# Optimization experiments

Hardware: AMD Instinct MI355X
Metric: run time of the kernel (lower is better)

## Reference

```python
import jax, jax.numpy as jnp
import numpy as np

N_HEADS = 2
WINDOW = 4
BLOCK = 256


def _get_rel_emb(emb, length):
    # emb: [1, 2*WINDOW+1, K] -> [1, 2*length-1, K]
    pad = max(length - (WINDOW + 1), 0)
    start = max((WINDOW + 1) - length, 0)
    e = jnp.pad(emb, ((0, 0), (pad, pad), (0, 0)))
    return e[:, start:start + 2 * length - 1]


def _rel_to_abs(x):
    # x: [b, h, l, 2l-1] -> [b, h, l, l] (skew trick)
    b, h, l, _ = x.shape
    x = jnp.pad(x, ((0, 0), (0, 0), (0, 0), (0, 1))).reshape(b, h, 2 * l * l)
    x = jnp.pad(x, ((0, 0), (0, 0), (0, l - 1))).reshape(b, h, l + 1, 2 * l - 1)
    return x[:, :, :l, l - 1:]


def _abs_to_rel(x):
    # x: [b, h, l, l] -> [b, h, l, 2l-1] (inverse skew)
    b, h, l, _ = x.shape
    x = jnp.pad(x, ((0, 0), (0, 0), (0, 0), (0, l - 1))).reshape(b, h, l * (2 * l - 1))
    x = jnp.pad(x, ((0, 0), (0, 0), (l, 0))).reshape(b, h, l, 2 * l)
    return x[:, :, :, 1:]


def _attention(x, c, attn_mask, Wq, bq, Wk, bk, Wv, bv, Wo, bo, emb_rel_k, emb_rel_v):
    B, C, T = x.shape
    H, K = N_HEADS, C // N_HEADS
    # projections (torch Linear on [B,T,C])
    q = (jnp.einsum('bct,cd->btd', x, Wq) + bq).reshape(B, T, H, K).transpose(0, 2, 1, 3)
    k = (jnp.einsum('bct,cd->btd', c, Wk) + bk).reshape(B, T, H, K).transpose(0, 2, 1, 3)
    v = (jnp.einsum('bct,cd->btd', c, Wv) + bv).reshape(B, T, H, K).transpose(0, 2, 1, 3)
    qs = q / jnp.sqrt(jnp.float32(K))
    scores = jnp.einsum('bhtk,bhsk->bhts', qs, k)  # [B,H,T,T]
    # relative-position key logits (heads_share=True -> single table)
    rel_k = _get_rel_emb(emb_rel_k, T)[0]          # [2T-1, K]
    rel_logits = jnp.einsum('bhtk,rk->bhtr', qs, rel_k)
    scores = scores + _rel_to_abs(rel_logits)
    # proximal bias: -log1p(|i-j|)
    r = jnp.arange(T, dtype=jnp.float32)
    scores = scores - jnp.log1p(jnp.abs(r[:, None] - r[None, :]))[None, None]
    # attn mask + block-local mask (block mask active because mask is given)
    ij = jnp.arange(T)
    block_ok = jnp.abs(ij[:, None] - ij[None, :]) <= BLOCK
    valid = (attn_mask != 0) & block_ok[None, None]
    scores = jnp.where(valid, scores, jnp.float32(-1e4))
    p = jax.nn.softmax(scores, axis=-1)
    out = jnp.einsum('bhts,bhsk->bhtk', p, v)
    # relative-position value contribution
    rel_v = _get_rel_emb(emb_rel_v, T)[0]          # [2T-1, K]
    out = out + jnp.einsum('bhtr,rk->bhtk', _abs_to_rel(p), rel_v)
    out = out.transpose(0, 2, 1, 3).reshape(B, T, C)
    y = jnp.einsum('btd,do->bto', out, Wo) + bo
    return y.transpose(0, 2, 1)  # [B, out_channels, T]


def setup_inputs() -> dict:
    key = jax.random.key(0)
    ks = jax.random.split(key, 8)
    B, C, T = 4, 192, 2048
    K = C // N_HEADS
    s = jnp.float32(0.05)
    rel_std = jnp.float32(K ** -0.5)
    return {
        'x': jax.random.normal(ks[0], (B, C, T), jnp.float32),
        'c': jax.random.normal(ks[1], (B, C, T), jnp.float32),
        'Wq': jax.random.normal(ks[2], (C, C), jnp.float32) * s,
        'bq': jnp.zeros((C,), jnp.float32),
        'Wk': jax.random.normal(ks[3], (C, C), jnp.float32) * s,
        'bk': jnp.zeros((C,), jnp.float32),
        'Wv': jax.random.normal(ks[4], (C, C), jnp.float32) * s,
        'bv': jnp.zeros((C,), jnp.float32),
        'Wo': jax.random.normal(ks[5], (C, C), jnp.float32) * s,
        'bo': jnp.zeros((C,), jnp.float32),
        'emb_rel_k': jax.random.normal(ks[6], (1, 2 * WINDOW + 1, K), jnp.float32) * rel_std,
        'emb_rel_v': jax.random.normal(ks[7], (1, 2 * WINDOW + 1, K), jnp.float32) * rel_std,
        'attn_mask': jnp.ones((B, 1, T, T), jnp.int32),
    }


def reference(x, c, Wq, bq, Wk, bk, Wv, bv, Wo, bo, emb_rel_k, emb_rel_v, attn_mask):
    return _attention(x, c, attn_mask, Wq, bq, Wk, bk, Wv, bv, Wo, bo, emb_rel_k, emb_rel_v)
```

## Files before the change

kernel.cpp:

```cpp
#include <hip/hip_runtime.h>
#include <hip/hip_bf16.h>

#define B_DIM 4
#define C_DIM 192
#define T_SEQ 2048
#define H_DIM 2
#define K_DIM 96
#define BAND 256
#define IT 16
#define NJT 34
#define WSLOT 544
#define WPD 556
#define PRS (2*WPD)
#define PMW 17
#define XSTR 200
#define OSTR 200
#define PDS 40

typedef __attribute__((ext_vector_type(8))) short bf16x8;
typedef __attribute__((ext_vector_type(4))) short bf16x4;
typedef __attribute__((ext_vector_type(4))) float f32x4;
#define MFMA16 __builtin_amdgcn_mfma_f32_16x16x32_bf16

__device__ __forceinline__ float bfbits2f(short s) {
    union { short s; __hip_bfloat16 h; } u; u.s = s; return __bfloat162float(u.h);
}
__device__ __forceinline__ short f2bf_bits(float f) {
    union { __hip_bfloat16 h; short s; } u; u.h = __float2bfloat16(f); return u.s;
}

#define OFF_WT(m)  ((size_t)(m)*73728)
#define OFF_BQS    ((size_t)294912)
#define OFF_RELKBF ((size_t)295680)
#define OFF_RVT    ((size_t)298752)
#define OFF_QBF    ((size_t)304896)
#define OFF_KBF    (OFF_QBF + 3145728)
#define OFF_VTB    (OFF_KBF + 3145728)

__device__ __forceinline__ int swz512(int hw) { return ((hw & 7) << 6) + (hw >> 3); }

__global__ __launch_bounds__(256)
void prep_kernel(const float* __restrict__ Wq, const float* __restrict__ Wk,
                 const float* __restrict__ Wv, const float* __restrict__ Wo,
                 const float* __restrict__ bq, const float* __restrict__ relk,
                 const float* __restrict__ relv, char* __restrict__ ws)
{
    const float qscale = 0.10206207261596577f;
    const int bidx = blockIdx.x;
    const int tid  = threadIdx.x;

    if (bidx < 576) {
        const size_t idx = (size_t)bidx*256 + tid;
        const int mi  = (int)(idx / 36864);
        const int rem = (int)(idx % 36864);
        const int c = rem / C_DIM, d = rem % C_DIM;
        const float* src = (mi == 0) ? Wq : (mi == 1) ? Wk : (mi == 2) ? Wv : Wo;
        float v = src[c*C_DIM + d];
        if (mi == 0) v *= qscale;
        ((short*)(ws + OFF_WT(mi)))[d*C_DIM + c] = f2bf_bits(v);
        return;
    }
    if (tid < C_DIM)
        ((float*)(ws + OFF_BQS))[tid] = bq[tid]*qscale;
    short* rkb = (short*)(ws + OFF_RELKBF);
    for (int idx = tid; idx < 16*K_DIM; idx += 256) {
        const int row = idx / K_DIM;
        rkb[idx] = (row < 9) ? f2bf_bits(relk[idx]) : (short)0;
    }
    short* rvt = (short*)(ws + OFF_RVT);
    for (int idx = tid; idx < K_DIM*32; idx += 256) {
        const int col = idx >> 5, dd = idx & 31;
        rvt[idx] = (dd < 9) ? f2bf_bits(relv[dd*K_DIM + col]) : (short)0;
    }
}

__global__ __launch_bounds__(256)
void proj_kernel(const float* __restrict__ x, const float* __restrict__ cin,
                 const float* __restrict__ bk, const float* __restrict__ bv,
                 char* __restrict__ ws)
{
    __shared__ short xs[IT*XSTR];
    __shared__ short cs[IT*XSTR];
    const int bid = swz512(blockIdx.x);
    const int b   = bid >> 7;
    const int t0  = (bid & 127) * IT;
    const int tid = threadIdx.x;
    const int wave = tid >> 6, lane = tid & 63;
    const int q4 = lane >> 4, lr = lane & 15;

    for (int l = tid; l < 768; l += 256) {
        const int cr = l >> 2, u = l & 3;
        const size_t off = (size_t)(b*C_DIM + cr)*T_SEQ + t0 + 4*u;
        const float4 xv = *reinterpret_cast<const float4*>(x + off);
        const float4 cv = *reinterpret_cast<const float4*>(cin + off);
        xs[(4*u+0)*XSTR + cr] = f2bf_bits(xv.x);
        xs[(4*u+1)*XSTR + cr] = f2bf_bits(xv.y);
        xs[(4*u+2)*XSTR + cr] = f2bf_bits(xv.z);
        xs[(4*u+3)*XSTR + cr] = f2bf_bits(xv.w);
        cs[(4*u+0)*XSTR + cr] = f2bf_bits(cv.x);
        cs[(4*u+1)*XSTR + cr] = f2bf_bits(cv.y);
        cs[(4*u+2)*XSTR + cr] = f2bf_bits(cv.z);
        cs[(4*u+3)*XSTR + cr] = f2bf_bits(cv.w);
    }
    __syncthreads();

    const short* WqT = (const short*)(ws + OFF_WT(0));
    const short* WkT = (const short*)(ws + OFF_WT(1));
    const short* WvT = (const short*)(ws + OFF_WT(2));

    f32x4 qa[3], ka[3], va[3];
    #pragma unroll
    for (int j = 0; j < 3; ++j) {
        qa[j] = (f32x4){0,0,0,0}; ka[j] = (f32x4){0,0,0,0}; va[j] = (f32x4){0,0,0,0};
    }
    for (int kc = 0; kc < 6; ++kc) {
        const int ko = kc*32 + q4*8;
        const bf16x8 xf = *reinterpret_cast<const bf16x8*>(xs + lr*XSTR + ko);
        const bf16x8 cf = *reinterpret_cast<const bf16x8*>(cs + lr*XSTR + ko);
        #pragma unroll
        for (int j = 0; j < 3; ++j) {
            const int dt = 3*wave + j;
            const bf16x8 wqf = *reinterpret_cast<const bf16x8*>(WqT + (dt*16 + lr)*C_DIM + ko);
            const bf16x8 wkf = *reinterpret_cast<const bf16x8*>(WkT + (dt*16 + lr)*C_DIM + ko);
            const bf16x8 wvf = *reinterpret_cast<const bf16x8*>(WvT + (dt*16 + lr)*C_DIM + ko);
            qa[j] = MFMA16(xf, wqf, qa[j], 0, 0, 0);
            ka[j] = MFMA16(cf, wkf, ka[j], 0, 0, 0);
            va[j] = MFMA16(wvf, cf, va[j], 0, 0, 0);
        }
    }

    const float* bqs = (const float*)(ws + OFF_BQS);
    short* qbf = (short*)(ws + OFF_QBF);
    short* kbf = (short*)(ws + OFF_KBF);
    short* vtb = (short*)(ws + OFF_VTB);
    #pragma unroll
    for (int j = 0; j < 3; ++j) {
        const int dt = 3*wave + j;
        {
            const int d = dt*16 + lr, h = d/K_DIM, kk = d%K_DIM;
            const int bh = b*H_DIM + h;
            const float bq_v = bqs[d], bk_v = bk[d];
            #pragma unroll
            for (int e = 0; e < 4; ++e) {
                const int t = t0 + q4*4 + e;
                const size_t off = ((size_t)bh*T_SEQ + t)*K_DIM + kk;
                qbf[off] = f2bf_bits(qa[j][e] + bq_v);
                kbf[off] = f2bf_bits(ka[j][e] + bk_v);
            }
        }
        {
            #pragma unroll
            for (int e = 0; e < 4; ++e) {
                const int d = dt*16 + q4*4 + e, h = d/K_DIM, kk = d%K_DIM;
                const int bh = b*H_DIM + h;
                vtb[((size_t)bh*K_DIM + kk)*T_SEQ + t0 + lr] = f2bf_bits(va[e == e ? j : j][e] + bv[d]);
            }
        }
    }
}

__global__ __launch_bounds__(512, 4)
void attn_oproj_kernel(const int* __restrict__ mask, const float* __restrict__ bo,
                       float* __restrict__ y, char* __restrict__ ws)
{
    __shared__ __align__(16) float ps[2*IT*WPD];
    __shared__ float lt[257];
    __shared__ __align__(16) char upool[2560];
    unsigned* pm_s = (unsigned*)upool;
    float*    rl   = (float*)(upool + 1088);
    short*    pd_s = (short*)upool;

    const short* qbf = (const short*)(ws + OFF_QBF);
    const short* kbf = (const short*)(ws + OFF_KBF);
    const short* vtb = (const short*)(ws + OFF_VTB);
    const short* rkb = (const short*)(ws + OFF_RELKBF);
    const short* rvt = (const short*)(ws + OFF_RVT);
    const short* WoT = (const short*)(ws + OFF_WT(3));

    const int bid = swz512(blockIdx.x);
    const int b   = bid >> 7;
    const int i0  = (bid & 127) * IT;
    const int tid = threadIdx.x;
    const int wave = tid >> 6, lane = tid & 63;
    const int head = wave >> 2, wv = wave & 3;
    const int q4 = lane >> 4, lr = lane & 15;

    const int jlo  = max(0, i0 - BAND);
    const int jhi  = min(T_SEQ - 1, i0 + IT - 1 + BAND);
    const int wlen = jhi - jlo + 1;
    const size_t qk_base = (size_t)(b*H_DIM + head) * T_SEQ * K_DIM;

    bf16x8 qa[3];
    {
        const short* qrow = qbf + qk_base + (size_t)(i0 + lr)*K_DIM + q4*8;
        #pragma unroll
        for (int kc = 0; kc < 3; ++kc)
            qa[kc] = *reinterpret_cast<const bf16x8*>(qrow + kc*32);
    }

    for (int idx = tid; idx < 257; idx += 512) lt[idx] = log1pf((float)idx);

    if (tid < IT*PMW) {
        const int r = tid / PMW, w = tid % PMW;
        const int* mrow = mask + ((size_t)b*T_SEQ + i0 + r)*T_SEQ;
        unsigned bits = 0;
        #pragma unroll
        for (int g4 = 0; g4 < 8; ++g4) {
            const int jg = jlo + 32*w + 4*g4;
            if (jg + 3 < T_SEQ) {
                const int4 mv = *reinterpret_cast<const int4*>(mrow + jg);
                bits |= (unsigned)(mv.x != 0) << (4*g4);
                bits |= (unsigned)(mv.y != 0) << (4*g4+1);
                bits |= (unsigned)(mv.z != 0) << (4*g4+2);
                bits |= (unsigned)(mv.w != 0) << (4*g4+3);
            } else {
                #pragma unroll
                for (int e = 0; e < 4; ++e)
                    if (jg + e < T_SEQ && mrow[jg+e] != 0) bits |= 1u << (4*g4+e);
            }
        }
        pm_s[tid] = bits;
    }

    float* psh = ps + head*(IT*WPD);
    {
        int jt = wv;
        int jr = jlo + jt*16 + lr; if (jr > T_SEQ-1) jr = T_SEQ-1;
        const short* kr = kbf + qk_base + (size_t)jr*K_DIM + q4*8;
        bf16x8 kf0 = *reinterpret_cast<const bf16x8*>(kr);
        bf16x8 kf1 = *reinterpret_cast<const bf16x8*>(kr + 32);
        bf16x8 kf2 = *reinterpret_cast<const bf16x8*>(kr + 64);
        while (true) {
            const int jn = jt + 4;
            const bool more = (jn < NJT);
            bf16x8 nf0, nf1, nf2;
            if (more) {
                int jr2 = jlo + jn*16 + lr; if (jr2 > T_SEQ-1) jr2 = T_SEQ-1;
                const short* kr2 = kbf + qk_base + (size_t)jr2*K_DIM + q4*8;
                nf0 = *reinterpret_cast<const bf16x8*>(kr2);
                nf1 = *reinterpret_cast<const bf16x8*>(kr2 + 32);
                nf2 = *reinterpret_cast<const bf16x8*>(kr2 + 64);
            }
            f32x4 s = {0.f,0.f,0.f,0.f};
            s = MFMA16(qa[0], kf0, s, 0, 0, 0);
            s = MFMA16(qa[1], kf1, s, 0, 0, 0);
            s = MFMA16(qa[2], kf2, s, 0, 0, 0);
            float* pr = psh + (q4*4)*WPD + jt*16 + lr;
            pr[0*WPD] = s[0]; pr[1*WPD] = s[1]; pr[2*WPD] = s[2]; pr[3*WPD] = s[3];
            if (!more) break;
            kf0 = nf0; kf1 = nf1; kf2 = nf2;
            jt = jn;
        }
    }
    if (wv == 3) {
        const short* krow = rkb + lr*K_DIM + q4*8;
        f32x4 rs = {0.f,0.f,0.f,0.f};
        #pragma unroll
        for (int kc = 0; kc < 3; ++kc)
            rs = MFMA16(qa[kc], *reinterpret_cast<const bf16x8*>(krow + kc*32), rs, 0, 0, 0);
        if (lr < 9) {
            #pragma unroll
            for (int e = 0; e < 4; ++e)
                rl[head*144 + (q4*4 + e)*9 + lr] = rs[e];
        }
    }
    __syncthreads();

    {
        const int rg = tid >> 4, sj = tid & 15;
        const int hh = rg >> 4, r = rg & 15;
        const int i = i0 + r;
        float* prow = ps + hh*(IT*WPD) + r*WPD;
        float vals[36];
        float m = -INFINITY;
        #pragma unroll
        for (int mm = 0; mm < 9; ++mm) {
            const int j0 = 4*sj + 64*mm;
            float4 pv = make_float4(0.f,0.f,0.f,0.f);
            unsigned mb = 0;
            if (j0 < WSLOT) {
                pv = *reinterpret_cast<const float4*>(prow + j0);
                mb = pm_s[r*PMW + (j0 >> 5)] >> (j0 & 31);
            }
            const float pe[4] = {pv.x, pv.y, pv.z, pv.w};
            #pragma unroll
            for (int e = 0; e < 4; ++e) {
                const int j = j0 + e;
                float val = -INFINITY;
                if (j0 < WSLOT && j < wlen) {
                    const int jg = jlo + j, dd = jg - i;
                    const int ad = dd < 0 ? -dd : dd;
                    if (ad <= BAND && ((mb >> e) & 1)) {
                        val = pe[e] - lt[ad];
                        if ((unsigned)(dd + 4) <= 8u) val += rl[hh*144 + r*9 + dd + 4];
                    }
                }
                vals[mm*4 + e] = val;
                m = fmaxf(m, val);
            }
        }
        #pragma unroll
        for (int off = 8; off > 0; off >>= 1) m = fmaxf(m, __shfl_xor(m, off, 64));
        if (m == -INFINITY) m = 0.f;
        float ssum = 0.f;
        #pragma unroll
        for (int u = 0; u < 36; ++u) { vals[u] = __expf(vals[u] - m); ssum += vals[u]; }
        #pragma unroll
        for (int off = 8; off > 0; off >>= 1) ssum += __shfl_xor(ssum, off, 64);
        const float inv = ssum > 0.f ? 1.f/ssum : 0.f;
        short* pbrow = (short*)prow;
        #pragma unroll
        for (int mm = 0; mm < 9; ++mm) {
            const int j0 = 4*sj + 64*mm;
            if (j0 < WSLOT) {
                bf16x4 w;
                #pragma unroll
                for (int e = 0; e < 4; ++e) w[e] = f2bf_bits(vals[mm*4+e]*inv);
                *reinterpret_cast<bf16x4*>(pbrow + j0) = w;
            }
        }
    }
    __syncthreads();

    for (int idx = tid; idx < 2*IT*PDS; idx += 512) {
        const int hh = idx / (IT*PDS), rem2 = idx % (IT*PDS);
        const int r = rem2 / PDS, kk = rem2 % PDS;
        short v = 0;
        if (kk < 9) {
            const int jg = i0 + r + kk - 4;
            if (jg >= 0 && jg < T_SEQ)
                v = ((const short*)ps)[hh*(IT*PRS) + r*PRS + (jg - jlo)];
        }
        pd_s[idx] = v;
    }

    const short* pbh = (const short*)ps + head*(IT*PRS);
    f32x4 o0 = {0.f,0.f,0.f,0.f}, o1 = {0.f,0.f,0.f,0.f};
    {
        const short* vbase0 = vtb + qk_base + (size_t)(wv*16 + lr)*T_SEQ;
        const short* vbase1 = vtb + qk_base + (size_t)((wv+4)*16 + lr)*T_SEQ;
        int tc = jlo + q4*8; if (tc > T_SEQ-8) tc = T_SEQ-8;
        bf16x8 vb0 = *reinterpret_cast<const bf16x8*>(vbase0 + tc);
        bf16x8 vb1 = {};
        if (wv < 2) vb1 = *reinterpret_cast<const bf16x8*>(vbase1 + tc);
        for (int kc = 0; kc < NJT/2; ++kc) {
            bf16x8 nv0, nv1;
            const bool more = (kc + 1 < NJT/2);
            if (more) {
                int tn = jlo + (kc+1)*32 + q4*8; if (tn > T_SEQ-8) tn = T_SEQ-8;
                nv0 = *reinterpret_cast<const bf16x8*>(vbase0 + tn);
                if (wv < 2) nv1 = *reinterpret_cast<const bf16x8*>(vbase1 + tn);
            }
            const bf16x8 pa = *reinterpret_cast<const bf16x8*>(pbh + lr*PRS + kc*32 + q4*8);
            o0 = MFMA16(pa, vb0, o0, 0, 0, 0);
            if (wv < 2) o1 = MFMA16(pa, vb1, o1, 0, 0, 0);
            if (more) { vb0 = nv0; if (wv < 2) vb1 = nv1; }
        }
    }
    __syncthreads();

    {
        const bf16x8 pda = *reinterpret_cast<const bf16x8*>(pd_s + head*(IT*PDS) + lr*PDS + q4*8);
        const bf16x8 rv0 = *reinterpret_cast<const bf16x8*>(rvt + (wv*16 + lr)*32 + q4*8);
        o0 = MFMA16(pda, rv0, o0, 0, 0, 0);
        if (wv < 2) {
            const bf16x8 rv1 = *reinterpret_cast<const bf16x8*>(rvt + ((wv+4)*16 + lr)*32 + q4*8);
            o1 = MFMA16(pda, rv1, o1, 0, 0, 0);
        }
    }

    {
        short* outs = (short*)ps;
        #pragma unroll
        for (int u = 0; u < 2; ++u) {
            if (u == 1 && wv >= 2) break;
            const int nt = u ? wv + 4 : wv;
            const f32x4 oc = u ? o1 : o0;
            const int col = head*K_DIM + nt*16 + lr;
            #pragma unroll
            for (int e = 0; e < 4; ++e)
                outs[(q4*4 + e)*OSTR + col] = f2bf_bits(oc[e]);
        }
    }
    __syncthreads();

    {
        const short* outs = (const short*)ps;
        #pragma unroll
        for (int u = 0; u < 2; ++u) {
            if (u == 1 && wave >= 4) break;
            const int dt = u ? wave + 8 : wave;
            f32x4 a = {0.f,0.f,0.f,0.f};
            #pragma unroll
            for (int kc = 0; kc < 6; ++kc) {
                const int ko = kc*32 + q4*8;
                const bf16x8 af = *reinterpret_cast<const bf16x8*>(
                    WoT + (size_t)(dt*16 + lr)*C_DIM + ko);
                const bf16x8 bfr = *reinterpret_cast<const bf16x8*>(outs + lr*OSTR + ko);
                a = MFMA16(af, bfr, a, 0, 0, 0);
            }
            #pragma unroll
            for (int e = 0; e < 4; ++e) {
                const int d = dt*16 + q4*4 + e;
                y[((size_t)b*C_DIM + d)*T_SEQ + i0 + lr] = a[e] + bo[d];
            }
        }
    }
}

extern "C" void kernel_launch(void* const* d_in, const int* in_sizes, int n_in,
                              void* d_out, int out_size, void* d_ws, size_t ws_size,
                              hipStream_t stream)
{
    const float* x    = (const float*)d_in[0];
    const float* c    = (const float*)d_in[1];
    const float* Wq   = (const float*)d_in[2];
    const float* bq   = (const float*)d_in[3];
    const float* Wk   = (const float*)d_in[4];
    const float* bk   = (const float*)d_in[5];
    const float* Wv   = (const float*)d_in[6];
    const float* bv   = (const float*)d_in[7];
    const float* Wo   = (const float*)d_in[8];
    const float* bo   = (const float*)d_in[9];
    const float* relk = (const float*)d_in[10];
    const float* relv = (const float*)d_in[11];
    const int*   mask = (const int*)d_in[12];
    float*       y    = (float*)d_out;
    char*        ws   = (char*)d_ws;

    hipLaunchKernelGGL(prep_kernel, dim3(577), dim3(256), 0, stream,
                       Wq, Wk, Wv, Wo, bq, relk, relv, ws);
    hipLaunchKernelGGL(proj_kernel, dim3(B_DIM*(T_SEQ/16)), dim3(256), 0, stream,
                       x, c, bk, bv, ws);
    hipLaunchKernelGGL(attn_oproj_kernel, dim3(B_DIM*(T_SEQ/IT)), dim3(512), 0, stream,
                       mask, bo, y, ws);
}
```

Baseline: 175.3 us.

## Split attention per head, separate output projection, and split QKV projection blocks

The fused attention plus output-projection kernel becomes a per-head attention kernel with 256 threads that writes bf16 head outputs to a workspace buffer, followed by a separate output-projection kernel. The QKV projection is split into three blocks per tile, one per matrix, which triples the grid and lowers per-block register use. Weight transposition in prep now goes through a shared-memory tile so global reads and writes are coalesced. The aim is more parallel blocks and better occupancy, at the cost of an extra launch and a round trip of the attention output through global memory.

Result: slower. 183.9 us (+4.9%).

```diff
diff --git a/kernel.cpp b/kernel.cpp
--- a/kernel.cpp
+++ b/kernel.cpp
@@ -14,7 +14,6 @@
 #define PRS (2*WPD)
 #define PMW 17
 #define XSTR 200
-#define OSTR 200
 #define PDS 40
 
 typedef __attribute__((ext_vector_type(8))) short bf16x8;
@@ -22,9 +21,6 @@
 typedef __attribute__((ext_vector_type(4))) float f32x4;
 #define MFMA16 __builtin_amdgcn_mfma_f32_16x16x32_bf16
 
-__device__ __forceinline__ float bfbits2f(short s) {
-    union { short s; __hip_bfloat16 h; } u; u.s = s; return __bfloat162float(u.h);
-}
 __device__ __forceinline__ short f2bf_bits(float f) {
     union { __hip_bfloat16 h; short s; } u; u.h = __float2bfloat16(f); return u.s;
 }
@@ -36,8 +32,7 @@
 #define OFF_QBF    ((size_t)304896)
 #define OFF_KBF    (OFF_QBF + 3145728)
 #define OFF_VTB    (OFF_KBF + 3145728)
-
-__device__ __forceinline__ int swz512(int hw) { return ((hw & 7) << 6) + (hw >> 3); }
+#define OFF_OBTC   (OFF_VTB + 3145728)
 
 __global__ __launch_bounds__(256)
 void prep_kernel(const float* __restrict__ Wq, const float* __restrict__ Wk,
@@ -49,15 +44,26 @@
     const int bidx = blockIdx.x;
     const int tid  = threadIdx.x;
 
-    if (bidx < 576) {
-        const size_t idx = (size_t)bidx*256 + tid;
-        const int mi  = (int)(idx / 36864);
-        const int rem = (int)(idx % 36864);
-        const int c = rem / C_DIM, d = rem % C_DIM;
+    if (bidx < 144) {
+        __shared__ float tile[32][33];
+        const int mi = bidx / 36, tl = bidx % 36;
+        const int R0 = (tl / 6) * 32, C0 = (tl % 6) * 32;
         const float* src = (mi == 0) ? Wq : (mi == 1) ? Wk : (mi == 2) ? Wv : Wo;
-        float v = src[c*C_DIM + d];
-        if (mi == 0) v *= qscale;
-        ((short*)(ws + OFF_WT(mi)))[d*C_DIM + c] = f2bf_bits(v);
+        const int r = tid >> 5, cc = tid & 31;
+        #pragma unroll
+        for (int i = 0; i < 4; ++i) {
+            const int rr = r + 8*i;
+            tile[rr][cc] = src[(R0 + rr)*C_DIM + C0 + cc];
+        }
+        __syncthreads();
+        short* dst = (short*)(ws + OFF_WT(mi));
+        #pragma unroll
+        for (int i = 0; i < 4; ++i) {
+            const int rr = r + 8*i;
+            float v = tile[cc][rr];
+            if (mi == 0) v *= qscale;
+            dst[(C0 + rr)*C_DIM + R0 + cc] = f2bf_bits(v);
+        }
         return;
     }
     if (tid < C_DIM)
@@ -74,98 +80,82 @@
     }
 }
 
-__global__ __launch_bounds__(256)
+__global__ __launch_bounds__(256, 6)
 void proj_kernel(const float* __restrict__ x, const float* __restrict__ cin,
                  const float* __restrict__ bk, const float* __restrict__ bv,
                  char* __restrict__ ws)
 {
-    __shared__ short xs[IT*XSTR];
-    __shared__ short cs[IT*XSTR];
-    const int bid = swz512(blockIdx.x);
-    const int b   = bid >> 7;
-    const int t0  = (bid & 127) * IT;
+    __shared__ short sb[IT*XSTR];
+    const int hw = blockIdx.x;
+    const int L  = (hw & 7)*192 + (hw >> 3);
+    const int which = L % 3;
+    const int rest  = L / 3;
+    const int b  = rest >> 7;
+    const int t0 = (rest & 127) * IT;
     const int tid = threadIdx.x;
     const int wave = tid >> 6, lane = tid & 63;
     const int q4 = lane >> 4, lr = lane & 15;
 
+    const float* src = (which == 0) ? x : cin;
     for (int l = tid; l < 768; l += 256) {
         const int cr = l >> 2, u = l & 3;
-        const size_t off = (size_t)(b*C_DIM + cr)*T_SEQ + t0 + 4*u;
-        const float4 xv = *reinterpret_cast<const float4*>(x + off);
-        const float4 cv = *reinterpret_cast<const float4*>(cin + off);
-        xs[(4*u+0)*XSTR + cr] = f2bf_bits(xv.x);
-        xs[(4*u+1)*XSTR + cr] = f2bf_bits(xv.y);
-        xs[(4*u+2)*XSTR + cr] = f2bf_bits(xv.z);
-        xs[(4*u+3)*XSTR + cr] = f2bf_bits(xv.w);
-        cs[(4*u+0)*XSTR + cr] = f2bf_bits(cv.x);
-        cs[(4*u+1)*XSTR + cr] = f2bf_bits(cv.y);
-        cs[(4*u+2)*XSTR + cr] = f2bf_bits(cv.z);
-        cs[(4*u+3)*XSTR + cr] = f2bf_bits(cv.w);
+        const float4 v4 = *reinterpret_cast<const float4*>(
+            src + (size_t)(b*C_DIM + cr)*T_SEQ + t0 + 4*u);
+        sb[(4*u+0)*XSTR + cr] = f2bf_bits(v4.x);
+        sb[(4*u+1)*XSTR + cr] = f2bf_bits(v4.y);
+        sb[(4*u+2)*XSTR + cr] = f2bf_bits(v4.z);
+        sb[(4*u+3)*XSTR + cr] = f2bf_bits(v4.w);
     }
     __syncthreads();
 
-    const short* WqT = (const short*)(ws + OFF_WT(0));
-    const short* WkT = (const short*)(ws + OFF_WT(1));
-    const short* WvT = (const short*)(ws + OFF_WT(2));
-
-    f32x4 qa[3], ka[3], va[3];
+    const short* WT = (const short*)(ws + OFF_WT(which));
+    f32x4 a[3];
     #pragma unroll
-    for (int j = 0; j < 3; ++j) {
-        qa[j] = (f32x4){0,0,0,0}; ka[j] = (f32x4){0,0,0,0}; va[j] = (f32x4){0,0,0,0};
-    }
+    for (int j = 0; j < 3; ++j) a[j] = (f32x4){0.f,0.f,0.f,0.f};
     for (int kc = 0; kc < 6; ++kc) {
         const int ko = kc*32 + q4*8;
-        const bf16x8 xf = *reinterpret_cast<const bf16x8*>(xs + lr*XSTR + ko);
-        const bf16x8 cf = *reinterpret_cast<const bf16x8*>(cs + lr*XSTR + ko);
+        const bf16x8 sf = *reinterpret_cast<const bf16x8*>(sb + lr*XSTR + ko);
         #pragma unroll
         for (int j = 0; j < 3; ++j) {
-            const int dt = 3*wave + j;
-            const bf16x8 wqf = *reinterpret_cast<const bf16x8*>(WqT + (dt*16 + lr)*C_DIM + ko);
-            const bf16x8 wkf = *reinterpret_cast<const bf16x8*>(WkT + (dt*16 + lr)*C_DIM + ko);
-            const bf16x8 wvf = *reinterpret_cast<const bf16x8*>(WvT + (dt*16 + lr)*C_DIM + ko);
-            qa[j] = MFMA16(xf, wqf, qa[j], 0, 0, 0);
-            ka[j] = MFMA16(cf, wkf, ka[j], 0, 0, 0);
-            va[j] = MFMA16(wvf, cf, va[j], 0, 0, 0);
+            const bf16x8 wf = *reinterpret_cast<const bf16x8*>(
+                WT + ((3*wave + j)*16 + lr)*C_DIM + ko);
+            a[j] = (which == 2) ? MFMA16(wf, sf, a[j], 0, 0, 0)
+                                : MFMA16(sf, wf, a[j], 0, 0, 0);
         }
     }
 
     const float* bqs = (const float*)(ws + OFF_BQS);
-    short* qbf = (short*)(ws + OFF_QBF);
-    short* kbf = (short*)(ws + OFF_KBF);
-    short* vtb = (short*)(ws + OFF_VTB);
     #pragma unroll
     for (int j = 0; j < 3; ++j) {
         const int dt = 3*wave + j;
-        {
+        if (which <= 1) {
             const int d = dt*16 + lr, h = d/K_DIM, kk = d%K_DIM;
             const int bh = b*H_DIM + h;
-            const float bq_v = bqs[d], bk_v = bk[d];
+            const float bias = (which == 0) ? bqs[d] : bk[d];
+            short* dst = (short*)(ws + (which == 0 ? OFF_QBF : OFF_KBF));
             #pragma unroll
             for (int e = 0; e < 4; ++e) {
                 const int t = t0 + q4*4 + e;
-                const size_t off = ((size_t)bh*T_SEQ + t)*K_DIM + kk;
-                qbf[off] = f2bf_bits(qa[j][e] + bq_v);
-                kbf[off] = f2bf_bits(ka[j][e] + bk_v);
-            }
-        }
-        {
+                dst[((size_t)bh*T_SEQ + t)*K_DIM + kk] = f2bf_bits(a[j][e] + bias);
+            }
+        } else {
+            short* vtb = (short*)(ws + OFF_VTB);
             #pragma unroll
             for (int e = 0; e < 4; ++e) {
                 const int d = dt*16 + q4*4 + e, h = d/K_DIM, kk = d%K_DIM;
                 const int bh = b*H_DIM + h;
-                vtb[((size_t)bh*K_DIM + kk)*T_SEQ + t0 + lr] = f2bf_bits(va[e == e ? j : j][e] + bv[d]);
-            }
-        }
-    }
-}
-
-__global__ __launch_bounds__(512, 4)
-void attn_oproj_kernel(const int* __restrict__ mask, const float* __restrict__ bo,
-                       float* __restrict__ y, char* __restrict__ ws)
+                vtb[((size_t)bh*K_DIM + kk)*T_SEQ + t0 + lr] = f2bf_bits(a[j][e] + bv[d]);
+            }
+        }
+    }
+}
+
+__global__ __launch_bounds__(256, 4)
+void attn_kernel(const int* __restrict__ mask, char* __restrict__ ws)
 {
-    __shared__ __align__(16) float ps[2*IT*WPD];
+    __shared__ __align__(16) float ps[IT*WPD];
     __shared__ float lt[257];
-    __shared__ __align__(16) char upool[2560];
+    __shared__ __align__(16) char upool[1664];
     unsigned* pm_s = (unsigned*)upool;
     float*    rl   = (float*)(upool + 1088);
     short*    pd_s = (short*)upool;
@@ -175,14 +165,15 @@
     const short* vtb = (const short*)(ws + OFF_VTB);
     const short* rkb = (const short*)(ws + OFF_RELKBF);
     const short* rvt = (const short*)(ws + OFF_RVT);
-    const short* WoT = (const short*)(ws + OFF_WT(3));
-
-    const int bid = swz512(blockIdx.x);
-    const int b   = bid >> 7;
-    const int i0  = (bid & 127) * IT;
+    short* obtc = (short*)(ws + OFF_OBTC);
+
+    const int L    = ((blockIdx.x & 7) << 7) + (blockIdx.x >> 3);
+    const int b    = L >> 8;
+    const int rem  = L & 255;
+    const int i0   = (rem >> 1) * IT;
+    const int head = rem & 1;
     const int tid = threadIdx.x;
     const int wave = tid >> 6, lane = tid & 63;
-    const int head = wave >> 2, wv = wave & 3;
     const int q4 = lane >> 4, lr = lane & 15;
 
     const int jlo  = max(0, i0 - BAND);
@@ -198,10 +189,10 @@
             qa[kc] = *reinterpret_cast<const bf16x8*>(qrow + kc*32);
     }
 
-    for (int idx = tid; idx < 257; idx += 512) lt[idx] = log1pf((float)idx);
-
-    if (tid < IT*PMW) {
-        const int r = tid / PMW, w = tid % PMW;
+    for (int idx = tid; idx < 257; idx += 256) lt[idx] = log1pf((float)idx);
+
+    for (int idx = tid; idx < IT*PMW; idx += 256) {
+        const int r = idx / PMW, w = idx % PMW;
         const int* mrow = mask + ((size_t)b*T_SEQ + i0 + r)*T_SEQ;
         unsigned bits = 0;
         #pragma unroll
@@ -219,12 +210,11 @@
                     if (jg + e < T_SEQ && mrow[jg+e] != 0) bits |= 1u << (4*g4+e);
             }
         }
-        pm_s[tid] = bits;
-    }
-
-    float* psh = ps + head*(IT*WPD);
+        pm_s[idx] = bits;
+    }
+
     {
-        int jt = wv;
+        int jt = wave;
         int jr = jlo + jt*16 + lr; if (jr > T_SEQ-1) jr = T_SEQ-1;
         const short* kr = kbf + qk_base + (size_t)jr*K_DIM + q4*8;
         bf16x8 kf0 = *reinterpret_cast<const bf16x8*>(kr);
@@ -245,14 +235,14 @@
             s = MFMA16(qa[0], kf0, s, 0, 0, 0);
             s = MFMA16(qa[1], kf1, s, 0, 0, 0);
             s = MFMA16(qa[2], kf2, s, 0, 0, 0);
-            float* pr = psh + (q4*4)*WPD + jt*16 + lr;
+            float* pr = ps + (q4*4)*WPD + jt*16 + lr;
             pr[0*WPD] = s[0]; pr[1*WPD] = s[1]; pr[2*WPD] = s[2]; pr[3*WPD] = s[3];
             if (!more) break;
             kf0 = nf0; kf1 = nf1; kf2 = nf2;
             jt = jn;
         }
     }
-    if (wv == 3) {
+    if (wave == 3) {
         const short* krow = rkb + lr*K_DIM + q4*8;
         f32x4 rs = {0.f,0.f,0.f,0.f};
         #pragma unroll
@@ -261,16 +251,15 @@
         if (lr < 9) {
             #pragma unroll
             for (int e = 0; e < 4; ++e)
-                rl[head*144 + (q4*4 + e)*9 + lr] = rs[e];
+                rl[(q4*4 + e)*9 + lr] = rs[e];
         }
     }
     __syncthreads();
 
     {
-        const int rg = tid >> 4, sj = tid & 15;
-        const int hh = rg >> 4, r = rg & 15;
+        const int r = tid >> 4, sj = tid & 15;
         const int i = i0 + r;
-        float* prow = ps + hh*(IT*WPD) + r*WPD;
+        float* prow = ps + r*WPD;
         float vals[36];
         float m = -INFINITY;
         #pragma unroll
@@ -292,7 +281,7 @@
                     const int ad = dd < 0 ? -dd : dd;
                     if (ad <= BAND && ((mb >> e) & 1)) {
                         val = pe[e] - lt[ad];
-                        if ((unsigned)(dd + 4) <= 8u) val += rl[hh*144 + r*9 + dd + 4];
+                        if ((unsigned)(dd + 4) <= 8u) val += rl[r*9 + dd + 4];
                     }
                 }
                 vals[mm*4 + e] = val;
@@ -322,88 +311,99 @@
     }
     __syncthreads();
 
-    for (int idx = tid; idx < 2*IT*PDS; idx += 512) {
-        const int hh = idx / (IT*PDS), rem2 = idx % (IT*PDS);
-        const int r = rem2 / PDS, kk = rem2 % PDS;
+    for (int idx = tid; idx < IT*PDS; idx += 256) {
+        const int r = idx / PDS, kk = idx % PDS;
         short v = 0;
         if (kk < 9) {
             const int jg = i0 + r + kk - 4;
             if (jg >= 0 && jg < T_SEQ)
-                v = ((const short*)ps)[hh*(IT*PRS) + r*PRS + (jg - jlo)];
+                v = ((const short*)ps)[r*PRS + (jg - jlo)];
         }
         pd_s[idx] = v;
     }
 
-    const short* pbh = (const short*)ps + head*(IT*PRS);
+    const short* pbh = (const short*)ps;
     f32x4 o0 = {0.f,0.f,0.f,0.f}, o1 = {0.f,0.f,0.f,0.f};
     {
-        const short* vbase0 = vtb + qk_base + (size_t)(wv*16 + lr)*T_SEQ;
-        const short* vbase1 = vtb + qk_base + (size_t)((wv+4)*16 + lr)*T_SEQ;
+        const short* vbase0 = vtb + qk_base + (size_t)(wave*16 + lr)*T_SEQ;
+        const short* vbase1 = vtb + qk_base + (size_t)((wave+4)*16 + lr)*T_SEQ;
         int tc = jlo + q4*8; if (tc > T_SEQ-8) tc = T_SEQ-8;
         bf16x8 vb0 = *reinterpret_cast<const bf16x8*>(vbase0 + tc);
         bf16x8 vb1 = {};
-        if (wv < 2) vb1 = *reinterpret_cast<const bf16x8*>(vbase1 + tc);
+        if (wave < 2) vb1 = *reinterpret_cast<const bf16x8*>(vbase1 + tc);
         for (int kc = 0; kc < NJT/2; ++kc) {
             bf16x8 nv0, nv1;
             const bool more = (kc + 1 < NJT/2);
             if (more) {
                 int tn = jlo + (kc+1)*32 + q4*8; if (tn > T_SEQ-8) tn = T_SEQ-8;
                 nv0 = *reinterpret_cast<const bf16x8*>(vbase0 + tn);
-                if (wv < 2) nv1 = *reinterpret_cast<const bf16x8*>(vbase1 + tn);
+                if (wave < 2) nv1 = *reinterpret_cast<const bf16x8*>(vbase1 + tn);
             }
             const bf16x8 pa = *reinterpret_cast<const bf16x8*>(pbh + lr*PRS + kc*32 + q4*8);
             o0 = MFMA16(pa, vb0, o0, 0, 0, 0);
-            if (wv < 2) o1 = MFMA16(pa, vb1, o1, 0, 0, 0);
-            if (more) { vb0 = nv0; if (wv < 2) vb1 = nv1; }
+            if (wave < 2) o1 = MFMA16(pa, vb1, o1, 0, 0, 0);
+            if (more) { vb0 = nv0; if (wave < 2) vb1 = nv1; }
         }
     }
     __syncthreads();
 
     {
-        const bf16x8 pda = *reinterpret_cast<const bf16x8*>(pd_s + head*(IT*PDS) + lr*PDS + q4*8);
-        const bf16x8 rv0 = *reinterpret_cast<const bf16x8*>(rvt + (wv*16 + lr)*32 + q4*8);
+        const bf16x8 pda = *reinterpret_cast<const bf16x8*>(pd_s + lr*PDS + q4*8);
+        const bf16x8 rv0 = *reinterpret_cast<const bf16x8*>(rvt + (wave*16 + lr)*32 + q4*8);
         o0 = MFMA16(pda, rv0, o0, 0, 0, 0);
-        if (wv < 2) {
-            const bf16x8 rv1 = *reinterpret_cast<const bf16x8*>(rvt + ((wv+4)*16 + lr)*32 + q4*8);
+        if (wave < 2) {
+            const bf16x8 rv1 = *reinterpret_cast<const bf16x8*>(rvt + ((wave+4)*16 + lr)*32 + q4*8);
             o1 = MFMA16(pda, rv1, o1, 0, 0, 0);
         }
     }
-
-    {
-        short* outs = (short*)ps;
-        #pragma unroll
-        for (int u = 0; u < 2; ++u) {
-            if (u == 1 && wv >= 2) break;
-            const int nt = u ? wv + 4 : wv;
-            const f32x4 oc = u ? o1 : o0;
-            const int col = head*K_DIM + nt*16 + lr;
-            #pragma unroll
-            for (int e = 0; e < 4; ++e)
-                outs[(q4*4 + e)*OSTR + col] = f2bf_bits(oc[e]);
-        }
-    }
-    __syncthreads();
-
-    {
-        const short* outs = (const short*)ps;
-        #pragma unroll
-        for (int u = 0; u < 2; ++u) {
-            if (u == 1 && wave >= 4) break;
-            const int dt = u ? wave + 8 : wave;
-            f32x4 a = {0.f,0.f,0.f,0.f};
-            #pragma unroll
-            for (int kc = 0; kc < 6; ++kc) {
-                const int ko = kc*32 + q4*8;
-                const bf16x8 af = *reinterpret_cast<const bf16x8*>(
-                    WoT + (size_t)(dt*16 + lr)*C_DIM + ko);
-                const bf16x8 bfr = *reinterpret_cast<const bf16x8*>(outs + lr*OSTR + ko);
-                a = MFMA16(af, bfr, a, 0, 0, 0);
-            }
-            #pragma unroll
-            for (int e = 0; e < 4; ++e) {
-                const int d = dt*16 + q4*4 + e;
-                y[((size_t)b*C_DIM + d)*T_SEQ + i0 + lr] = a[e] + bo[d];
-            }
+    #pragma unroll
+    for (int u = 0; u < 2; ++u) {
+        if (u == 1 && wave >= 2) break;
+        const int nt = u ? wave + 4 : wave;
+        const f32x4 oc = u ? o1 : o0;
+        const int col = head*K_DIM + nt*16 + lr;
+        #pragma unroll
+        for (int e = 0; e < 4; ++e) {
+            const int i = i0 + q4*4 + e;
+            obtc[((size_t)b*T_SEQ + i)*C_DIM + col] = f2bf_bits(oc[e]);
+        }
+    }
+}
+
+__global__ __launch_bounds__(256)
+void oproj_kernel(const float* __restrict__ bo, float* __restrict__ y,
+                  const char* __restrict__ ws)
+{
+    const int bid = ((blockIdx.x & 7) << 6) + (blockIdx.x >> 3);
+    const int b   = bid >> 7;
+    const int t0  = (bid & 127) * 16;
+    const int tid = threadIdx.x;
+    const int wave = tid >> 6, lane = tid & 63;
+    const int q4 = lane >> 4, lr = lane & 15;
+
+    const short* WoT  = (const short*)(ws + OFF_WT(3));
+    const short* obtc = (const short*)(ws + OFF_OBTC);
+
+    f32x4 a[3];
+    #pragma unroll
+    for (int j = 0; j < 3; ++j) a[j] = (f32x4){0.f,0.f,0.f,0.f};
+    for (int kc = 0; kc < 6; ++kc) {
+        const int ko = kc*32 + q4*8;
+        const bf16x8 bf = *reinterpret_cast<const bf16x8*>(
+            obtc + ((size_t)b*T_SEQ + t0 + lr)*C_DIM + ko);
+        #pragma unroll
+        for (int j = 0; j < 3; ++j) {
+            const bf16x8 af = *reinterpret_cast<const bf16x8*>(
+                WoT + ((3*wave + j)*16 + lr)*C_DIM + ko);
+            a[j] = MFMA16(af, bf, a[j], 0, 0, 0);
+        }
+    }
+    #pragma unroll
+    for (int j = 0; j < 3; ++j) {
+        #pragma unroll
+        for (int e = 0; e < 4; ++e) {
+            const int d = (3*wave + j)*16 + q4*4 + e;
+            y[((size_t)b*C_DIM + d)*T_SEQ + t0 + lr] = a[j][e] + bo[d];
         }
     }
 }
@@ -428,10 +428,12 @@
     float*       y    = (float*)d_out;
     char*        ws   = (char*)d_ws;
 
-    hipLaunchKernelGGL(prep_kernel, dim3(577), dim3(256), 0, stream,
+    hipLaunchKernelGGL(prep_kernel, dim3(145), dim3(256), 0, stream,
                        Wq, Wk, Wv, Wo, bq, relk, relv, ws);
-    hipLaunchKernelGGL(proj_kernel, dim3(B_DIM*(T_SEQ/16)), dim3(256), 0, stream,
+    hipLaunchKernelGGL(proj_kernel, dim3(B_DIM*(T_SEQ/16)*3), dim3(256), 0, stream,
                        x, c, bk, bv, ws);
-    hipLaunchKernelGGL(attn_oproj_kernel, dim3(B_DIM*(T_SEQ/IT)), dim3(512), 0, stream,
-                       mask, bo, y, ws);
-}
+    hipLaunchKernelGGL(attn_kernel, dim3(B_DIM*H_DIM*(T_SEQ/IT)), dim3(256), 0, stream,
+                       mask, ws);
+    hipLaunchKernelGGL(oproj_kernel, dim3(B_DIM*(T_SEQ/16)), dim3(256), 0, stream,
+                       bo, y, ws);
+}
```
